# Performance work log

Hardware: AMD Instinct MI355X
Metric: run time of the kernel (lower is better)

## Reference

```python
import jax, jax.numpy as jnp
import numpy as np

B, T, D = 2, 2048, 1024
H = 16
HD = D // H  # head dim == config.k == config.v == 64


def setup_inputs() -> dict:
    key = jax.random.key(0)
    k1, k2, k3 = jax.random.split(key, 3)
    scale = 0.02
    x = jax.random.normal(k1, (B, T, D), dtype=jnp.float32)
    W1 = jax.random.normal(k2, (D, 3 * D), dtype=jnp.float32) * scale
    b1 = jnp.zeros((3 * D,), dtype=jnp.float32)
    W2 = jax.random.normal(k3, (D, D), dtype=jnp.float32) * scale
    b2 = jnp.zeros((D,), dtype=jnp.float32)
    return {"x": x, "W1": W1, "b1": b1, "W2": W2, "b2": b2}


def reference(x, W1, b1, W2, b2):
    # Fused QKV projection (dropout layers are identity in eval mode).
    Bx, Tx, C = x.shape
    qkv = x @ W1 + b1                      # [B, T, 3D]
    q, k, v = jnp.split(qkv, 3, axis=-1)   # each [B, T, D]
    q = q.reshape(Bx, Tx, H, HD).transpose(0, 2, 1, 3)  # [B, H, T, hd]
    k = k.reshape(Bx, Tx, H, HD).transpose(0, 2, 1, 3)
    v = v.reshape(Bx, Tx, H, HD).transpose(0, 2, 1, 3)

    logits = jnp.einsum('bhmk,bhnk->bhmn', q, k) / jnp.sqrt(jnp.float32(HD))
    # causal mask (lower-triangular bias buffer)
    causal = jnp.tril(jnp.ones((Tx, Tx), dtype=bool))
    logits = jnp.where(causal[None, None], logits, jnp.float32(-jnp.inf))
    att = jax.nn.softmax(logits, axis=-1)   # [B, H, T, T]

    y = jnp.einsum('bhmn,bhnv->bhmv', att, v)        # [B, H, T, hd]
    y = y.transpose(0, 2, 1, 3).reshape(Bx, Tx, C)   # [B, T, D]
    return y @ W2 + b2
```

## Files before the change

### kernel.cpp

```cpp
#include <hip/hip_runtime.h>

typedef __attribute__((ext_vector_type(8))) short bf16x8;
typedef __attribute__((ext_vector_type(4))) float f32x4;
typedef __attribute__((ext_vector_type(16))) float f32x16;
typedef __attribute__((ext_vector_type(4))) short short4v;
typedef __attribute__((ext_vector_type(4))) unsigned int uint4v;

#define B_  2
#define T_  2048
#define D_  1024
#define H_  16
#define HD_ 64

__device__ inline short f2bf(float f){
  unsigned u = __builtin_bit_cast(unsigned, f);
  u += 0x7fff + ((u >> 16) & 1);
  return (short)(u >> 16);
}

__device__ inline void gl2lds16(const void* g, void* l){
  __builtin_amdgcn_global_load_lds(
      (const __attribute__((address_space(1))) unsigned int*)g,
      (__attribute__((address_space(3))) unsigned int*)l, 16, 0, 0);
}

__global__ __launch_bounds__(256) void convert_f32_bf16(
    const float* __restrict__ in, short* __restrict__ out){
  int i = (blockIdx.x * 256 + threadIdx.x) * 4;
  float4 v = *(const float4*)(in + i);
  short4v o;
  o[0] = f2bf(v.x); o[1] = f2bf(v.y); o[2] = f2bf(v.z); o[3] = f2bf(v.w);
  *(short4v*)(out + i) = o;
}

__global__ __launch_bounds__(256) void transpose_f32_bf16(
    const float* __restrict__ in, short* __restrict__ out, int R, int C){
  __shared__ float tile[32][33];
  int tx = threadIdx.x & 31, ty0 = threadIdx.x >> 5;
  int bx = blockIdx.x << 5, by = blockIdx.y << 5;
#pragma unroll
  for (int i = 0; i < 4; i++){
    int ty = ty0 + i * 8;
    tile[ty][tx] = in[(by + ty) * C + bx + tx];
  }
  __syncthreads();
#pragma unroll
  for (int i = 0; i < 4; i++){
    int ty = ty0 + i * 8;
    out[(bx + ty) * R + by + tx] = f2bf(tile[tx][ty]);
  }
}

#define BM 128
#define BN 128
#define BK 32

#define QSCALE 0.18033688011112042f

template<int N_, int K_, int EPI>
__global__ __launch_bounds__(256) void gemm_bt(
    const short* __restrict__ A, const short* __restrict__ Bt,
    const float* __restrict__ bias,
    short* __restrict__ q, short* __restrict__ kk, short* __restrict__ vT,
    float* __restrict__ outf){
  __shared__ short As[2][BM * BK];
  __shared__ short Bs[2][BN * BK];
  const int tid = threadIdx.x;
  const int lane = tid & 63, w = tid >> 6;
  const int wm = w >> 1, wn = w & 1;
  const int lr = lane & 15, lk = lane >> 4;
  const int brow = blockIdx.y * BM, bcol = blockIdx.x * BN;
  f32x4 acc[4][4] = {};
  const short* Ag = A  + brow * K_;
  const short* Bg = Bt + bcol * K_;

  auto stage = [&](int buf, int k0){
#pragma unroll
    for (int i = 0; i < 2; i++){
      int idx = i * 256 + tid;
      int row = idx >> 2, c8 = (idx & 3) * 8;
      gl2lds16(Ag + row * K_ + k0 + c8, (char*)As[buf] + idx * 16);
      gl2lds16(Bg + row * K_ + k0 + c8, (char*)Bs[buf] + idx * 16);
    }
  };

  const int NT = K_ / BK;
  stage(0, 0);
  for (int t = 0; t < NT; ++t){
    const int cur = t & 1;
    if (t + 1 < NT){
      stage(cur ^ 1, (t + 1) * BK);
      asm volatile("s_waitcnt vmcnt(4)" ::: "memory");
    } else {
      asm volatile("s_waitcnt vmcnt(0)" ::: "memory");
    }
    __builtin_amdgcn_s_barrier();
    __builtin_amdgcn_sched_barrier(0);

    bf16x8 a[4], b[4];
#pragma unroll
    for (int mf = 0; mf < 4; mf++)
      a[mf] = *(const bf16x8*)(As[cur] + (wm * 64 + mf * 16 + lr) * BK + lk * 8);
#pragma unroll
    for (int nf = 0; nf < 4; nf++)
      b[nf] = *(const bf16x8*)(Bs[cur] + (wn * 64 + nf * 16 + lr) * BK + lk * 8);
    __builtin_amdgcn_s_setprio(1);
#pragma unroll
    for (int mf = 0; mf < 4; mf++)
#pragma unroll
      for (int nf = 0; nf < 4; nf++)
        acc[mf][nf] = __builtin_amdgcn_mfma_f32_16x16x32_bf16(a[mf], b[nf], acc[mf][nf], 0, 0, 0);
    __builtin_amdgcn_s_setprio(0);
    __builtin_amdgcn_sched_barrier(0);
    __builtin_amdgcn_s_barrier();
  }

  if constexpr (EPI == 0){
#pragma unroll
    for (int nf = 0; nf < 4; nf++){
      int n = bcol + wn * 64 + nf * 16 + lr;
      float bv = bias[n];
      int sec = n >> 10, d = n & 1023, h = d >> 6, hd = d & 63;
#pragma unroll
      for (int mf = 0; mf < 4; mf++){
        int m0 = brow + wm * 64 + mf * 16 + lk * 4;
        int b = m0 >> 11, t0 = m0 & 2047;
        int bh = b * H_ + h;
        if (sec == 0){
#pragma unroll
          for (int r = 0; r < 4; r++)
            q[(bh * T_ + t0 + r) * HD_ + hd] = f2bf((acc[mf][nf][r] + bv) * QSCALE);
        } else if (sec == 1){
#pragma unroll
          for (int r = 0; r < 4; r++)
            kk[(bh * T_ + t0 + r) * HD_ + hd] = f2bf(acc[mf][nf][r] + bv);
        } else {
          float v0 = acc[mf][nf][0] + bv, v1 = acc[mf][nf][1] + bv;
          float v2 = acc[mf][nf][2] + bv, v3 = acc[mf][nf][3] + bv;
          unsigned lo = (unsigned)(unsigned short)f2bf(v0) | ((unsigned)(unsigned short)f2bf(v1) << 16);
          unsigned hi = (unsigned)(unsigned short)f2bf(v2) | ((unsigned)(unsigned short)f2bf(v3) << 16);
          uint2 pk; pk.x = lo; pk.y = hi;
          *(uint2*)(vT + (bh * HD_ + hd) * T_ + t0) = pk;
        }
      }
    }
  } else {
#pragma unroll
    for (int nf = 0; nf < 4; nf++){
      int n = bcol + wn * 64 + nf * 16 + lr;
      float bv = bias[n];
#pragma unroll
      for (int mf = 0; mf < 4; mf++){
        int m0 = brow + wm * 64 + mf * 16 + lk * 4;
#pragma unroll
        for (int r = 0; r < 4; r++)
          outf[(m0 + r) * N_ + n] = acc[mf][nf][r] + bv;
      }
    }
  }
}

__device__ inline int crow(int r, int h){ return (r & 3) + 8 * (r >> 2) + 4 * h; }

template<int SPLIT>
__global__ __launch_bounds__(256, 4) void attn32(
    const short* __restrict__ Q, const short* __restrict__ Kg,
    const short* __restrict__ Vt, short* __restrict__ Y,
    float* __restrict__ Op, float* __restrict__ ml){
  __shared__ short Ks[2][64 * 64];
  __shared__ short Vs[2][64 * 64];
  __shared__ float bounce[4][32];
  const int tid = threadIdx.x;
  const int w = tid >> 6, l = tid & 63;
  const int lq = l & 31, h = l >> 5;
  const int bx = blockIdx.x;
  int i, hf;
  if constexpr (SPLIT){
    int u = bx >> 5, v = u & 15;
    i = (v < 8) ? 15 - v : v - 8;
    hf = u >> 4;
  } else {
    i = (bx < 256) ? 15 - (bx >> 5) : (bx >> 5) - 8;
    hf = 0;
  }
  const int bh = bx & 31;
  const int q0 = i * 128, qw = q0 + w * 32;
  const int t0 = (SPLIT && hf) ? (i + 1) : 0;
  const int t1 = (SPLIT && !hf) ? (i + 1) : 2 * (i + 1);

  bf16x8 qb[4];
  {
    const short* qbase = Q + (bh * T_ + qw + lq) * HD_;
#pragma unroll
    for (int dk = 0; dk < 4; dk++)
      qb[dk] = *(const bf16x8*)(qbase + dk * 16 + h * 8);
  }

  f32x16 o0 = {}, o1 = {};
  float m = -1e30f, ll = 0.f;

  auto stage = [&](int buf, int t){
#pragma unroll
    for (int j = 0; j < 2; j++){
      int idx = j * 256 + tid;
      int row = idx >> 3, cb = (idx & 7) * 16;
      int cbs = cb ^ ((row & 7) << 4);
      gl2lds16(Kg + (bh * T_ + t * 64 + row) * HD_ + (cbs >> 1), (char*)Ks[buf] + idx * 16);
      gl2lds16(Vt + (bh * HD_ + row) * T_ + t * 64 + (cbs >> 1), (char*)Vs[buf] + idx * 16);
    }
  };

  stage(0, t0);
  for (int t = t0; t < t1; ++t){
    const int cur = (t - t0) & 1;
    if (t + 1 < t1){
      stage(cur ^ 1, t + 1);
      asm volatile("s_waitcnt vmcnt(4)" ::: "memory");
    } else {
      asm volatile("s_waitcnt vmcnt(0)" ::: "memory");
    }
    __builtin_amdgcn_s_barrier();
    __builtin_amdgcn_sched_barrier(0);

    const int kvb = t * 64;
    if (kvb <= qw + 31){
      const short* Kc = Ks[cur];
      const short* Vc = Vs[cur];

      f32x16 s[2] = {};
      __builtin_amdgcn_s_setprio(1);
#pragma unroll
      for (int kb = 0; kb < 2; kb++){
        int row = kb * 32 + lq;
        const char* rp = (const char*)Kc + row * 128;
        int swz = (row & 7) << 4;
#pragma unroll
        for (int dk = 0; dk < 4; dk++){
          bf16x8 ka = *(const bf16x8*)(rp + ((dk * 32 + h * 16) ^ swz));
          s[kb] = __builtin_amdgcn_mfma_f32_32x32x16_bf16(ka, qb[dk], s[kb], 0, 0, 0);
        }
      }
      __builtin_amdgcn_s_setprio(0);

      const int qg = qw + lq;
      if (kvb + 63 > qw){
#pragma unroll
        for (int kb = 0; kb < 2; kb++)
#pragma unroll
          for (int r = 0; r < 16; r++){
            int kv = kvb + kb * 32 + crow(r, h);
            if (kv > qg) s[kb][r] = -1e30f;
          }
      }

      float pm = s[0][0];
#pragma unroll
      for (int r = 1; r < 16; r++) pm = fmaxf(pm, s[0][r]);
#pragma unroll
      for (int r = 0; r < 16; r++) pm = fmaxf(pm, s[1][r]);
      pm = fmaxf(pm, __shfl_xor(pm, 32));

      if (__any(pm > m + 8.f)){
        float mn = fmaxf(pm, m);
        float sf = __builtin_amdgcn_exp2f(m - mn);
        m = mn;
        ll *= sf;
        bounce[w][lq] = sf;
#pragma unroll
        for (int r = 0; r < 16; r++){
          float sr = bounce[w][crow(r, h)];
          o0[r] *= sr; o1[r] *= sr;
        }
      }

      float ts = 0.f;
#pragma unroll
      for (int kb = 0; kb < 2; kb++)
#pragma unroll
        for (int r = 0; r < 16; r++){
          float p = __builtin_amdgcn_exp2f(s[kb][r] - m);
          s[kb][r] = p;
          ts += p;
        }
      ts += __shfl_xor(ts, 32);
      ll += ts;

      unsigned pw0[8], pw1[8];
#pragma unroll
      for (int kb = 0; kb < 2; kb++)
#pragma unroll
        for (int gg = 0; gg < 4; gg++){
          unsigned r0, r1;
          asm("v_cvt_pk_bf16_f32 %0, %1, %2" : "=v"(r0) : "v"(s[kb][gg * 4 + 0]), "v"(s[kb][gg * 4 + 1]));
          asm("v_cvt_pk_bf16_f32 %0, %1, %2" : "=v"(r1) : "v"(s[kb][gg * 4 + 2]), "v"(s[kb][gg * 4 + 3]));
          pw0[kb * 4 + gg] = r0;
          pw1[kb * 4 + gg] = r1;
        }
#pragma unroll
      for (int ks = 0; ks < 4; ks++){
        asm("v_permlane32_swap_b32 %0, %1" : "+v"(pw0[2 * ks]), "+v"(pw0[2 * ks + 1]));
        asm("v_permlane32_swap_b32 %0, %1" : "+v"(pw1[2 * ks]), "+v"(pw1[2 * ks + 1]));
      }

      __builtin_amdgcn_s_setprio(1);
#pragma unroll
      for (int ks = 0; ks < 4; ks++){
        uint4v paw;
        paw[0] = pw0[2 * ks];     paw[1] = pw1[2 * ks];
        paw[2] = pw0[2 * ks + 1]; paw[3] = pw1[2 * ks + 1];
        bf16x8 pa = __builtin_bit_cast(bf16x8, paw);
#pragma unroll
        for (int nb = 0; nb < 2; nb++){
          int row = nb * 32 + lq;
          bf16x8 vb = *(const bf16x8*)((const char*)Vc + row * 128 +
                        ((ks * 32 + h * 16) ^ ((row & 7) << 4)));
          if (nb == 0) o0 = __builtin_amdgcn_mfma_f32_32x32x16_bf16(pa, vb, o0, 0, 0, 0);
          else         o1 = __builtin_amdgcn_mfma_f32_32x32x16_bf16(pa, vb, o1, 0, 0, 0);
        }
      }
      __builtin_amdgcn_s_setprio(0);
    }
    __builtin_amdgcn_sched_barrier(0);
    __builtin_amdgcn_s_barrier();
  }

  if constexpr (SPLIT){
    float* Oq = Op + ((size_t)(hf * 32 + bh)) * (size_t)T_ * 64;
    if (h == 0){
      float* mlr = ml + ((size_t)(hf * 32 + bh) * T_ + (qw + lq)) * 2;
      mlr[0] = m; mlr[1] = ll;
    }
#pragma unroll
    for (int r = 0; r < 16; r++){
      int qg = qw + crow(r, h);
      Oq[qg * 64 + lq]      = o0[r];
      Oq[qg * 64 + 32 + lq] = o1[r];
    }
  } else {
    bounce[w][lq] = __builtin_amdgcn_rcpf(ll);
    const int b = bh >> 4, hh = bh & 15;
#pragma unroll
    for (int r = 0; r < 16; r++){
      int row = crow(r, h);
      float rl = bounce[w][row];
      int qg = qw + row;
      short* yb = Y + (b * T_ + qg) * D_ + hh * 64;
      yb[lq]      = f2bf(o0[r] * rl);
      yb[32 + lq] = f2bf(o1[r] * rl);
    }
  }
}

__global__ __launch_bounds__(256) void attn_merge(
    const float* __restrict__ Op, const float* __restrict__ ml,
    short* __restrict__ Y){
  int gid = blockIdx.x * 256 + threadIdx.x;
  int rid = gid >> 2, c16 = (gid & 3) * 16;
  float m1 = ml[rid * 2],           l1 = ml[rid * 2 + 1];
  float m2 = ml[131072 + rid * 2],  l2 = ml[131072 + rid * 2 + 1];
  float M  = fmaxf(m1, m2);
  float f1 = __builtin_amdgcn_exp2f(m1 - M);
  float f2 = __builtin_amdgcn_exp2f(m2 - M);
  float rl = 1.f / (f1 * l1 + f2 * l2);
  f1 *= rl; f2 *= rl;
  const float4* O1 = (const float4*)(Op + (size_t)rid * 64 + c16);
  const float4* O2 = (const float4*)(Op + 4194304ull + (size_t)rid * 64 + c16);
  int bh = rid >> 11, t = rid & 2047;
  short* yb = Y + (((bh >> 4) * T_ + t) * D_) + (bh & 15) * 64 + c16;
#pragma unroll
  for (int j = 0; j < 4; j++){
    float4 a = O1[j], b = O2[j];
    short4v o;
    o[0] = f2bf(f1 * a.x + f2 * b.x);
    o[1] = f2bf(f1 * a.y + f2 * b.y);
    o[2] = f2bf(f1 * a.z + f2 * b.z);
    o[3] = f2bf(f1 * a.w + f2 * b.w);
    *(short4v*)(yb + j * 4) = o;
  }
}

extern "C" void kernel_launch(void* const* d_in, const int* in_sizes, int n_in,
                              void* d_out, int out_size, void* d_ws, size_t ws_size,
                              hipStream_t stream) {
  const float* x  = (const float*)d_in[0];
  const float* W1 = (const float*)d_in[1];
  const float* b1 = (const float*)d_in[2];
  const float* W2 = (const float*)d_in[3];
  const float* b2 = (const float*)d_in[4];
  float* out = (float*)d_out;

  char* ws = (char*)d_ws;
  short* W1T = (short*)(ws);
  short* W2T = (short*)(ws + 6291456);
  short* xb  = (short*)(ws + 8388608);
  short* q   = (short*)(ws + 16777216);
  short* kk  = (short*)(ws + 25165824);
  short* vT  = (short*)(ws + 33554432);
  float* Op  = (float*)(ws + 41943040);
  float* mlb = (float*)(ws + 41943040 + 33554432);
  short* y   = xb;

  const size_t need = 41943040ull + 33554432ull + 1048576ull;
  const bool split = ws_size >= need;

  convert_f32_bf16<<<dim3(4096), dim3(256), 0, stream>>>(x, xb);
  transpose_f32_bf16<<<dim3(96, 32), dim3(256), 0, stream>>>(W1, W1T, 1024, 3072);
  transpose_f32_bf16<<<dim3(32, 32), dim3(256), 0, stream>>>(W2, W2T, 1024, 1024);
  gemm_bt<3072, 1024, 0><<<dim3(24, 32), dim3(256), 0, stream>>>(xb, W1T, b1, q, kk, vT, nullptr);
  if (split){
    attn32<1><<<dim3(1024), dim3(256), 0, stream>>>(q, kk, vT, nullptr, Op, mlb);
    attn_merge<<<dim3(1024), dim3(256), 0, stream>>>(Op, mlb, y);
  } else {
    attn32<0><<<dim3(512), dim3(256), 0, stream>>>(q, kk, vT, y, nullptr, nullptr);
  }
  gemm_bt<1024, 1024, 1><<<dim3(8, 32), dim3(256), 0, stream>>>(y, W2T, b2, nullptr, nullptr, nullptr, out);
}
```

Measured before the change: 123.4 us.

## Fuse prep kernels into one launch and widen QKV GEMM tile to 128x256

Merges the x conversion and two weight transposes into a single prep kernel dispatched by block index, removing two kernel launches. The QKV projection GEMM is templated on tile width and thread count and now uses 512-thread blocks computing 128x256 tiles, with adjusted load distribution and vmcnt waits. This raises B-tile reuse per block but halves the grid to 384 blocks, which may underfill the GPU. The launch_bounds occupancy hint of 4 blocks could also constrain registers.

```diff
diff --git a/kernel.cpp b/kernel.cpp
--- a/kernel.cpp
+++ b/kernel.cpp
@@ -24,20 +24,11 @@
       (__attribute__((address_space(3))) unsigned int*)l, 16, 0, 0);
 }
 
-__global__ __launch_bounds__(256) void convert_f32_bf16(
-    const float* __restrict__ in, short* __restrict__ out){
-  int i = (blockIdx.x * 256 + threadIdx.x) * 4;
-  float4 v = *(const float4*)(in + i);
-  short4v o;
-  o[0] = f2bf(v.x); o[1] = f2bf(v.y); o[2] = f2bf(v.z); o[3] = f2bf(v.w);
-  *(short4v*)(out + i) = o;
-}
-
-__global__ __launch_bounds__(256) void transpose_f32_bf16(
-    const float* __restrict__ in, short* __restrict__ out, int R, int C){
+__device__ inline void transpose_tile(const float* __restrict__ in,
+                                      short* __restrict__ out,
+                                      int R, int C, int bx, int by){
   __shared__ float tile[32][33];
   int tx = threadIdx.x & 31, ty0 = threadIdx.x >> 5;
-  int bx = blockIdx.x << 5, by = blockIdx.y << 5;
 #pragma unroll
   for (int i = 0; i < 4; i++){
     int ty = ty0 + i * 8;
@@ -51,35 +42,62 @@
   }
 }
 
+__global__ __launch_bounds__(256) void prep(
+    const float* __restrict__ x,  short* __restrict__ xb,
+    const float* __restrict__ W1, short* __restrict__ W1T,
+    const float* __restrict__ W2, short* __restrict__ W2T){
+  const int bid = blockIdx.x;
+  if (bid < 4096){
+    int i = (bid * 256 + threadIdx.x) * 4;
+    float4 v = *(const float4*)(x + i);
+    short4v o;
+    o[0] = f2bf(v.x); o[1] = f2bf(v.y); o[2] = f2bf(v.z); o[3] = f2bf(v.w);
+    *(short4v*)(xb + i) = o;
+  } else if (bid < 4096 + 3072){
+    int tb = bid - 4096;
+    transpose_tile(W1, W1T, 1024, 3072, (tb % 96) << 5, (tb / 96) << 5);
+  } else {
+    int tb = bid - 7168;
+    transpose_tile(W2, W2T, 1024, 1024, (tb % 32) << 5, (tb / 32) << 5);
+  }
+}
+
 #define BM 128
-#define BN 128
 #define BK 32
 
 #define QSCALE 0.18033688011112042f
 
-template<int N_, int K_, int EPI>
-__global__ __launch_bounds__(256) void gemm_bt(
+template<int N_, int K_, int EPI, int BN_, int TPB>
+__global__ __launch_bounds__(TPB, 4) void gemm_bt(
     const short* __restrict__ A, const short* __restrict__ Bt,
     const float* __restrict__ bias,
     short* __restrict__ q, short* __restrict__ kk, short* __restrict__ vT,
     float* __restrict__ outf){
+  constexpr int NWX = BN_ / 64;
+  constexpr int LA  = (BM * 64) / (TPB * 16);
+  constexpr int LB  = (BN_ * 64) / (TPB * 16);
   __shared__ short As[2][BM * BK];
-  __shared__ short Bs[2][BN * BK];
+  __shared__ short Bs[2][BN_ * BK];
   const int tid = threadIdx.x;
   const int lane = tid & 63, w = tid >> 6;
-  const int wm = w >> 1, wn = w & 1;
+  const int wm = w / NWX, wn = w % NWX;
   const int lr = lane & 15, lk = lane >> 4;
-  const int brow = blockIdx.y * BM, bcol = blockIdx.x * BN;
+  const int brow = blockIdx.y * BM, bcol = blockIdx.x * BN_;
   f32x4 acc[4][4] = {};
   const short* Ag = A  + brow * K_;
   const short* Bg = Bt + bcol * K_;
 
   auto stage = [&](int buf, int k0){
 #pragma unroll
-    for (int i = 0; i < 2; i++){
-      int idx = i * 256 + tid;
+    for (int i = 0; i < LA; i++){
+      int idx = i * TPB + tid;
       int row = idx >> 2, c8 = (idx & 3) * 8;
       gl2lds16(Ag + row * K_ + k0 + c8, (char*)As[buf] + idx * 16);
+    }
+#pragma unroll
+    for (int i = 0; i < LB; i++){
+      int idx = i * TPB + tid;
+      int row = idx >> 2, c8 = (idx & 3) * 8;
       gl2lds16(Bg + row * K_ + k0 + c8, (char*)Bs[buf] + idx * 16);
     }
   };
@@ -90,7 +108,10 @@
     const int cur = t & 1;
     if (t + 1 < NT){
       stage(cur ^ 1, (t + 1) * BK);
-      asm volatile("s_waitcnt vmcnt(4)" ::: "memory");
+      if constexpr (LA + LB == 3)
+        asm volatile("s_waitcnt vmcnt(3)" ::: "memory");
+      else
+        asm volatile("s_waitcnt vmcnt(4)" ::: "memory");
     } else {
       asm volatile("s_waitcnt vmcnt(0)" ::: "memory");
     }
@@ -403,15 +424,13 @@
   const size_t need = 41943040ull + 33554432ull + 1048576ull;
   const bool split = ws_size >= need;
 
-  convert_f32_bf16<<<dim3(4096), dim3(256), 0, stream>>>(x, xb);
-  transpose_f32_bf16<<<dim3(96, 32), dim3(256), 0, stream>>>(W1, W1T, 1024, 3072);
-  transpose_f32_bf16<<<dim3(32, 32), dim3(256), 0, stream>>>(W2, W2T, 1024, 1024);
-  gemm_bt<3072, 1024, 0><<<dim3(24, 32), dim3(256), 0, stream>>>(xb, W1T, b1, q, kk, vT, nullptr);
+  prep<<<dim3(8192), dim3(256), 0, stream>>>(x, xb, W1, W1T, W2, W2T);
+  gemm_bt<3072, 1024, 0, 256, 512><<<dim3(12, 32), dim3(512), 0, stream>>>(xb, W1T, b1, q, kk, vT, nullptr);
   if (split){
     attn32<1><<<dim3(1024), dim3(256), 0, stream>>>(q, kk, vT, nullptr, Op, mlb);
     attn_merge<<<dim3(1024), dim3(256), 0, stream>>>(Op, mlb, y);
   } else {
     attn32<0><<<dim3(512), dim3(256), 0, stream>>>(q, kk, vT, y, nullptr, nullptr);
   }
-  gemm_bt<1024, 1024, 1><<<dim3(8, 32), dim3(256), 0, stream>>>(y, W2T, b2, nullptr, nullptr, nullptr, out);
-}
+  gemm_bt<1024, 1024, 1, 128, 256><<<dim3(8, 32), dim3(256), 0, stream>>>(y, W2T, b2, nullptr, nullptr, nullptr, out);
+}
```

After: 117.8 us. 4.5% less time.
